# Optimization experiments

Measured on AMD Instinct MI355X. Metric: run time of the kernel, lower is better.

Reference implementation:

```python
import jax, jax.numpy as jnp
import numpy as np

NB = 32          # num_basis
RMAX = 2.5       # max_radius
M0, M1 = 16, 8   # multiplicities of 0e and 1o irreps

# normalize2mom constant for silu (makes E[act(x)^2]=1 under N(0,1)), as in e3nn FullyConnectedNet
_p, _w = np.polynomial.hermite_e.hermegauss(128)
_s = _p / (1.0 + np.exp(-_p))
SILU_C = float(1.0 / np.sqrt((_w * _s * _s).sum() / np.sqrt(2.0 * np.pi)))

INV3 = 1.0 / np.sqrt(3.0)   # w3j(1,1,0)=w3j(0,1,1)=w3j(1,0,1) coefficient
INV6 = 1.0 / np.sqrt(6.0)   # w3j(1,1,1) = eps_ijk/sqrt(6)
PW0 = float(np.sqrt(1.0 / (M0 + M1)))        # path weight -> 0e (component/element norm)
PW1 = float(np.sqrt(3.0 / (M0 + M1 + M1)))   # path weight -> 1o
PW_SIM = float(np.sqrt(1.0 / (M0 * M0 + M1 * M1)))  # similarity TP path weight


def basis_net(rb, W1, W2):
    # e3nn FullyConnectedNet([NB,16,numel], silu): x@W/sqrt(fan_in), normalized act, linear out
    h = SILU_C * jax.nn.silu(rb @ (W1 / np.sqrt(NB)))
    return h @ (W2 / np.sqrt(16.0))


def fc_tp(x0, x1, sh0, sh1, w):
    # FullyConnectedTensorProduct (16x0e+8x1o) x (0e+1o) -> (16x0e+8x1o), per-edge weights
    # x0 [E,16], x1 [E,8,3], sh0 [E], sh1 [E,3], w [E,640]
    E = w.shape[0]
    w0 = w[:, 0:256].reshape(E, M0, M0)    # 0e x 0e -> 0e
    w1 = w[:, 256:384].reshape(E, M0, M1)  # 0e x 1o -> 1o
    w2 = w[:, 384:448].reshape(E, M1, M1)  # 1o x 0e -> 1o
    w3 = w[:, 448:576].reshape(E, M1, M0)  # 1o x 1o -> 0e
    w4 = w[:, 576:640].reshape(E, M1, M1)  # 1o x 1o -> 1o
    dot = jnp.einsum('eui,ei->eu', x1, sh1)
    out0 = PW0 * (jnp.einsum('euw,eu->ew', w0, x0 * sh0[:, None])
                  + INV3 * jnp.einsum('euw,eu->ew', w3, dot))
    crx = jnp.cross(x1, sh1[:, None, :])
    out1 = PW1 * (INV3 * jnp.einsum('euw,eu,ei->ewi', w1, x0, sh1)
                  + INV3 * sh0[:, None, None] * jnp.einsum('euw,eui->ewi', w2, x1)
                  + INV6 * jnp.einsum('euw,eui->ewi', w4, crx))
    return out0, out1


def forward(x, pos, edge_src, edge_dst, w_key1, w_key2, w_val1, w_val2, w_q0, w_q1, w_sim0, w_sim1):
    N = x.shape[0]
    x0 = x[:, :M0]                       # [N,16] scalars
    x1 = x[:, M0:].reshape(N, M1, 3)     # [N,8,3] vectors
    vec = pos[edge_src] - pos[edge_dst]  # [E,3]
    r = jnp.sqrt((vec * vec).sum(-1) + 1e-12)
    # bessel soft_one_hot_linspace with cutoff, scaled by sqrt(num_basis)
    n = jnp.arange(1, NB + 1, dtype=x.dtype) * jnp.pi
    rb = jnp.sqrt(2.0 / RMAX) * jnp.sin(n * (r[:, None] / RMAX)) / r[:, None]
    rb = jnp.where(r[:, None] < RMAX, rb, 0.0) * np.sqrt(1.0 * NB)
    # spherical harmonics lmax=1, normalize=True, normalization='component'
    unit = vec / r[:, None]
    sh0 = jnp.ones_like(r)
    sh1 = np.sqrt(3.0) * unit
    # query projection (o3.Linear, per-irrep dense / sqrt(fan_in))
    q0 = x0 @ (w_q0 / np.sqrt(M0))
    q1 = jnp.einsum('nui,uv->nvi', x1, w_q1) / np.sqrt(M1)
    x0s, x1s = x0[edge_src], x1[edge_src]
    k0, k1 = fc_tp(x0s, x1s, sh0, sh1, basis_net(rb, w_key1, w_key2))
    v0, v1 = fc_tp(x0s, x1s, sh0, sh1, basis_net(rb, w_val1, w_val2))
    # similarity TP (q,k)->0e
    s = PW_SIM * (jnp.einsum('eu,uv,ev->e', q0[edge_dst], w_sim0, k0)
                  + INV3 * jnp.einsum('eui,uv,evi->e', q1[edge_dst], w_sim1, k1))
    # scatter softmax over incoming edges per dst node
    smax = jax.ops.segment_max(s, edge_dst, num_segments=N)
    ex = jnp.exp(s - smax[edge_dst])
    attn = ex / jax.ops.segment_sum(ex, edge_dst, num_segments=N)[edge_dst]
    coef = jnp.sqrt(jax.nn.relu(attn))
    vals = jnp.concatenate([v0, v1.reshape(-1, 3 * M1)], axis=-1)  # [E,40]
    return jax.ops.segment_sum(coef[:, None] * vals, edge_dst, num_segments=N)


def setup_inputs() -> dict:
    key = jax.random.key(0)
    ks = jax.random.split(key, 12)
    N, E = 16384, 262144
    return dict(
        x=jax.random.normal(ks[0], (N, 40), jnp.float32),
        pos=jax.random.uniform(ks[1], (N, 3), jnp.float32) * 2.0,  # box so r spans cutoff
        edge_src=jax.random.randint(ks[2], (E,), 0, N, jnp.int32),
        edge_dst=jax.random.randint(ks[3], (E,), 0, N, jnp.int32),
        w_key1=jax.random.normal(ks[4], (32, 16), jnp.float32),
        w_key2=jax.random.normal(ks[5], (16, 640), jnp.float32),
        w_val1=jax.random.normal(ks[6], (32, 16), jnp.float32),
        w_val2=jax.random.normal(ks[7], (16, 640), jnp.float32),
        w_q0=jax.random.normal(ks[8], (16, 16), jnp.float32),
        w_q1=jax.random.normal(ks[9], (8, 8), jnp.float32),
        w_sim0=jax.random.normal(ks[10], (16, 16), jnp.float32),
        w_sim1=jax.random.normal(ks[11], (8, 8), jnp.float32),
    )


def reference(x, pos, edge_src, edge_dst, w_key1, w_key2, w_val1, w_val2, w_q0, w_q1, w_sim0, w_sim1):
    return forward(x, pos, edge_src, edge_dst, w_key1, w_key2, w_val1, w_val2, w_q0, w_q1, w_sim0, w_sim1)
```

## Files before the change

### kernel.cpp

```cpp
#include <hip/hip_runtime.h>
#include <math.h>

#define TPB 256
#define TPBF 192
#define SRCS_PER_GRP 8
#define SRC_STRIDE_U16 1928

#define RMAX_F 2.5f
#define PI_F 3.14159265358979323846f
#define SQRT3_F 1.7320508075688772f
#define INV3_F 0.5773502691896258f
#define INV6_F 0.4082482904638631f
#define PW0_F 0.2041241452319315f
#define PW1_F 0.3061862178478972f
#define PWSIM_F 0.05590169943749474f
#define SILU_C_F 1.676866f
#define RB_F 0.8944271909999159f
#define INV_SQRT8_F 0.35355339059327373f

typedef unsigned short u16t;
typedef _Float16 f16x2 __attribute__((ext_vector_type(2)));

#if defined(__has_builtin)
#if __has_builtin(__builtin_amdgcn_fdot2)
#define HAVE_FDOT2 1
#else
#define HAVE_FDOT2 0
#endif
#else
#define HAVE_FDOT2 0
#endif


__device__ __forceinline__ unsigned f2bf(float f) {
  unsigned b = __float_as_uint(f);
  return (b + 0x7fffu + ((b >> 16) & 1u)) >> 16;
}
__device__ __forceinline__ float bf2f(unsigned s) {
  return __uint_as_float(s << 16);
}

__device__ __forceinline__ f16x2 as_f16x2(int v) {
  union { int i; f16x2 h; } u; u.i = v; return u.h;
}

__device__ __forceinline__ float dot2f16(f16x2 a, f16x2 b, float c) {
#if HAVE_FDOT2
  return __builtin_amdgcn_fdot2(a, b, c, false);
#else
  return fmaf((float)a.x, (float)b.x, fmaf((float)a.y, (float)b.y, c));
#endif
}

__device__ __forceinline__ float dotjh(const u16t* __restrict__ t,
                                       const f16x2* __restrict__ hp) {
  const int4* q = reinterpret_cast<const int4*>(t);
  int4 a = q[0], b = q[1];
  float s0 = 0.f, s1 = 0.f;
  s0 = dot2f16(as_f16x2(a.x), hp[0], s0);
  s1 = dot2f16(as_f16x2(a.y), hp[1], s1);
  s0 = dot2f16(as_f16x2(a.z), hp[2], s0);
  s1 = dot2f16(as_f16x2(a.w), hp[3], s1);
  s0 = dot2f16(as_f16x2(b.x), hp[4], s0);
  s1 = dot2f16(as_f16x2(b.y), hp[5], s1);
  s0 = dot2f16(as_f16x2(b.z), hp[6], s0);
  s1 = dot2f16(as_f16x2(b.w), hp[7], s1);
  return s0 + s1;
}

__device__ __forceinline__ void pack_h16(const float* __restrict__ h,
                                         f16x2* __restrict__ hp) {
#pragma unroll
  for (int i = 0; i < 8; ++i) {
    f16x2 v;
    v.x = (_Float16)h[2 * i + 0];
    v.y = (_Float16)h[2 * i + 1];
    hp[i] = v;
  }
}

__device__ __forceinline__ float dot16u(const float* __restrict__ w, const float* __restrict__ h) {
  float a0 = 0.f, a1 = 0.f, a2 = 0.f, a3 = 0.f;
#pragma unroll
  for (int j = 0; j < 16; j += 4) {
    a0 = fmaf(h[j + 0], w[j + 0], a0);
    a1 = fmaf(h[j + 1], w[j + 1], a1);
    a2 = fmaf(h[j + 2], w[j + 2], a2);
    a3 = fmaf(h[j + 3], w[j + 3], a3);
  }
  return (a0 + a1) + (a2 + a3);
}

__device__ __forceinline__ void compute_h2s(const float* __restrict__ pos,
                                            const float* __restrict__ W1k,
                                            const float* __restrict__ W1v,
                                            int src, int dst,
                                            float& shx, float& shy, float& shz,
                                            float hk[16], float hv[16]) {
  float vx = pos[3 * src + 0] - pos[3 * dst + 0];
  float vy = pos[3 * src + 1] - pos[3 * dst + 1];
  float vz = pos[3 * src + 2] - pos[3 * dst + 2];
  float r2 = fmaf(vx, vx, fmaf(vy, vy, vz * vz)) + 1e-12f;
  float r = sqrtf(r2);
  float inv_r = 1.0f / r;
  shx = SQRT3_F * vx * inv_r;
  shy = SQRT3_F * vy * inv_r;
  shz = SQRT3_F * vz * inv_r;
  float f = (r < RMAX_F) ? (RB_F * inv_r) : 0.0f;
  float t0 = (PI_F / RMAX_F) * r;
  float s1, c1;
  __sincosf(t0, &s1, &c1);
  float c2 = 2.0f * c1;
  float sm = 0.0f, sc = s1;
  float ak[16], av[16];
#pragma unroll
  for (int j = 0; j < 16; ++j) { ak[j] = 0.0f; av[j] = 0.0f; }
#pragma unroll 2
  for (int n = 0; n < 32; ++n) {
    float rb = f * sc;
    const float* wk = W1k + n * 16;
    const float* wv = W1v + n * 16;
#pragma unroll
    for (int j = 0; j < 16; ++j) ak[j] = fmaf(rb, wk[j], ak[j]);
#pragma unroll
    for (int j = 0; j < 16; ++j) av[j] = fmaf(rb, wv[j], av[j]);
    float nx = fmaf(c2, sc, -sm);
    sm = sc; sc = nx;
  }
#pragma unroll
  for (int j = 0; j < 16; ++j) {
    float v = ak[j];
    hk[j] = SILU_C_F * v * (1.0f / (1.0f + __expf(-v)));
    float w = av[j];
    hv[j] = SILU_C_F * w * (1.0f / (1.0f + __expf(-w)));
  }
}

__device__ __forceinline__ void gen_entry(const float* __restrict__ W2T,
                                          const float* __restrict__ xr,
                                          int mm, float out[16]) {
#pragma unroll
  for (int j = 0; j < 16; ++j) out[j] = 0.f;
  if (mm < 16) {
    int w = mm;
#pragma unroll 1
    for (int u = 0; u < 16; ++u) {
      float xu = xr[u];
      const float* wp = W2T + (u * 16 + w) * 16;
#pragma unroll
      for (int j = 0; j < 16; ++j) out[j] = fmaf(xu, wp[j], out[j]);
    }
  } else if (mm < 24) {
    int w = mm - 16;
#pragma unroll 1
    for (int u = 0; u < 16; ++u) {
      float xu = xr[u];
      const float* wp = W2T + (256 + u * 8 + w) * 16;
#pragma unroll
      for (int j = 0; j < 16; ++j) out[j] = fmaf(xu, wp[j], out[j]);
    }
  } else if (mm < 48) {
    int tt = mm - 24, w = tt / 3, i = tt - w * 3;
#pragma unroll 1
    for (int u = 0; u < 8; ++u) {
      float xu = xr[16 + u * 3 + i];
      const float* wp = W2T + (384 + u * 8 + w) * 16;
#pragma unroll
      for (int j = 0; j < 16; ++j) out[j] = fmaf(xu, wp[j], out[j]);
    }
  } else if (mm < 96) {
    int tt = mm - 48, w = tt / 3, i = tt - w * 3;
#pragma unroll 1
    for (int u = 0; u < 8; ++u) {
      float xu = xr[16 + u * 3 + i];
      const float* wp = W2T + (448 + u * 16 + w) * 16;
#pragma unroll
      for (int j = 0; j < 16; ++j) out[j] = fmaf(xu, wp[j], out[j]);
    }
  } else {
    int tt = mm - 96, w = tt / 3, i = tt - w * 3;
#pragma unroll 1
    for (int u = 0; u < 8; ++u) {
      float xu = xr[16 + u * 3 + i];
      const float* wp = W2T + (576 + u * 8 + w) * 16;
#pragma unroll
      for (int j = 0; j < 16; ++j) out[j] = fmaf(xu, wp[j], out[j]);
    }
  }
}

__device__ __forceinline__ void gen_tables(const float* __restrict__ W2T,
                                           const float* __restrict__ xsh,
                                           u16t* __restrict__ tl,
                                           int nsrc, int tid) {
  for (int idx = tid; idx < nsrc * 120; idx += TPBF) {
    int m, s;
    if (nsrc == SRCS_PER_GRP) {
      m = idx >> 3;
      s = idx & 7;
    } else {
      m = idx / nsrc;
      s = idx - m * nsrc;
    }
    float out[16];
    gen_entry(W2T, xsh + s * 40, m, out);
    unsigned r[8];
#pragma unroll
    for (int k = 0; k < 8; ++k) {
      union { f16x2 h; unsigned u; } cv;
      cv.h.x = (_Float16)out[2 * k + 0];
      cv.h.y = (_Float16)out[2 * k + 1];
      r[k] = cv.u;
    }
    int4* dp = reinterpret_cast<int4*>(&tl[s * SRC_STRIDE_U16 + m * 16]);
    dp[0] = make_int4((int)r[0], (int)r[1], (int)r[2], (int)r[3]);
    dp[1] = make_int4((int)r[4], (int)r[5], (int)r[6], (int)r[7]);
  }
}


__global__ void k_prep(const float* __restrict__ wk2, const float* __restrict__ wv2,
                       const float* __restrict__ wq0, const float* __restrict__ wq1,
                       const float* __restrict__ ws0, const float* __restrict__ ws1,
                       float* __restrict__ W2Tk, float* __restrict__ W2Tv,
                       float* __restrict__ C0, float* __restrict__ C1) {
  int i = blockIdx.x * blockDim.x + threadIdx.x;
  if (i < 10240) {
    int o = i >> 4, j = i & 15;
    W2Tk[i] = wk2[j * 640 + o] * 0.25f;
  } else if (i < 20480) {
    int k = i - 10240;
    int o = k >> 4, j = k & 15;
    W2Tv[k] = wv2[j * 640 + o] * 0.25f;
  } else if (i < 20736) {
    int k = i - 20480;
    int t = k >> 4, v = k & 15;
    float a = 0.f;
#pragma unroll
    for (int u = 0; u < 16; ++u) a = fmaf(wq0[t * 16 + u] * 0.25f, ws0[u * 16 + v], a);
    C0[k] = a;
  } else if (i < 20800) {
    int k = i - 20736;
    int t = k >> 3, v = k & 7;
    float a = 0.f;
#pragma unroll
    for (int u = 0; u < 8; ++u) a = fmaf(wq1[t * 8 + u] * INV_SQRT8_F, ws1[u * 8 + v], a);
    C1[k] = a;
  }
}

__global__ void k_node(const float* __restrict__ x, const float* __restrict__ C0,
                       const float* __restrict__ C1, float* __restrict__ qs0g,
                       float* __restrict__ qs1g, int N) {
  int n = blockIdx.x * blockDim.x + threadIdx.x;
  if (n >= N) return;
  float xr[40];
  const float4* p = reinterpret_cast<const float4*>(x + (size_t)n * 40);
#pragma unroll
  for (int q = 0; q < 10; ++q) {
    float4 v = p[q];
    xr[q * 4 + 0] = v.x; xr[q * 4 + 1] = v.y; xr[q * 4 + 2] = v.z; xr[q * 4 + 3] = v.w;
  }
  float o0[16];
#pragma unroll
  for (int v = 0; v < 16; ++v) o0[v] = 0.f;
#pragma unroll
  for (int t = 0; t < 16; ++t) {
    float xt = xr[t];
    const float* c = C0 + t * 16;
#pragma unroll
    for (int v = 0; v < 16; ++v) o0[v] = fmaf(xt, c[v], o0[v]);
  }
  float4* q0p = reinterpret_cast<float4*>(qs0g + (size_t)n * 16);
#pragma unroll
  for (int q = 0; q < 4; ++q)
    q0p[q] = make_float4(o0[q * 4], o0[q * 4 + 1], o0[q * 4 + 2], o0[q * 4 + 3]);

  float o1[24];
#pragma unroll
  for (int v = 0; v < 24; ++v) o1[v] = 0.f;
#pragma unroll
  for (int u = 0; u < 8; ++u) {
    const float* c = C1 + u * 8;
    float xa = xr[16 + u * 3 + 0], xb = xr[16 + u * 3 + 1], xc = xr[16 + u * 3 + 2];
#pragma unroll
    for (int v = 0; v < 8; ++v) {
      float cv = c[v];
      o1[v * 3 + 0] = fmaf(xa, cv, o1[v * 3 + 0]);
      o1[v * 3 + 1] = fmaf(xb, cv, o1[v * 3 + 1]);
      o1[v * 3 + 2] = fmaf(xc, cv, o1[v * 3 + 2]);
    }
  }
  float4* q1p = reinterpret_cast<float4*>(qs1g + (size_t)n * 24);
#pragma unroll
  for (int q = 0; q < 6; ++q)
    q1p[q] = make_float4(o1[q * 4], o1[q * 4 + 1], o1[q * 4 + 2], o1[q * 4 + 3]);
}


__global__ void k_hist2(const int* __restrict__ esrc, const int* __restrict__ edst,
                        int* __restrict__ cnt_s, int* __restrict__ cnt_d, int E) {
  int e = blockIdx.x * blockDim.x + threadIdx.x;
  if (e < E) {
    atomicAdd(&cnt_s[esrc[e]], 1);
    atomicAdd(&cnt_d[edst[e]], 1);
  }
}

__global__ void k_hist1(const int* __restrict__ key, int* __restrict__ cnt, int E) {
  int e = blockIdx.x * blockDim.x + threadIdx.x;
  if (e < E) atomicAdd(&cnt[key[e]], 1);
}

__global__ __launch_bounds__(1024) void k_scan2(const int* __restrict__ cnt_s,
                                                int* __restrict__ off_s,
                                                int* __restrict__ cur_s,
                                                const int* __restrict__ cnt_d,
                                                int* __restrict__ off_d,
                                                int* __restrict__ cur_d, int N) {
  const int* __restrict__ cnt = blockIdx.x ? cnt_d : cnt_s;
  int* __restrict__ off = blockIdx.x ? off_d : off_s;
  int* __restrict__ cur = blockIdx.x ? cur_d : cur_s;
  __shared__ int ls[1024];
  int tid = threadIdx.x;
  int per = (N + 1023) >> 10;
  int base = tid * per;
  int sum = 0;
  for (int j = 0; j < per; ++j) {
    int idx = base + j;
    if (idx < N) sum += cnt[idx];
  }
  ls[tid] = sum;
  __syncthreads();
  for (int d = 1; d < 1024; d <<= 1) {
    int v = (tid >= d) ? ls[tid - d] : 0;
    __syncthreads();
    ls[tid] += v;
    __syncthreads();
  }
  int run = ls[tid] - sum;
  for (int j = 0; j < per; ++j) {
    int idx = base + j;
    if (idx < N) {
      off[idx] = run;
      cur[idx] = run;
      run += cnt[idx];
    }
  }
  if (tid == 1023) off[N] = run;
}

__global__ void k_place(const int* __restrict__ key, int* __restrict__ cursor,
                        int* __restrict__ perm, int E) {
  int e = blockIdx.x * blockDim.x + threadIdx.x;
  if (e < E) {
    int p = atomicAdd(&cursor[key[e]], 1);
    perm[p] = e;
  }
}

__global__ void k_idx_dst(const int* __restrict__ perm, const int* __restrict__ edst,
                          int* __restrict__ cursor, int* __restrict__ idx, int E) {
  int p = blockIdx.x * blockDim.x + threadIdx.x;
  if (p < E) {
    int q = atomicAdd(&cursor[edst[perm[p]]], 1);
    idx[q] = p;
  }
}


__global__ __launch_bounds__(TPBF) void k_fused(
    const float* __restrict__ x, const float* __restrict__ pos,
    const int* __restrict__ esrc, const int* __restrict__ edst,
    const int* __restrict__ perm, const int* __restrict__ off_s,
    const float* __restrict__ W1k, const float* __restrict__ W2Tk,
    const float* __restrict__ W1v, const float* __restrict__ W2Tv,
    const float* __restrict__ qs0g, const float* __restrict__ qs1g,
    float* __restrict__ s_out, u16t* __restrict__ stg, int N) {
  __shared__ __align__(16) u16t tl[SRCS_PER_GRP * SRC_STRIDE_U16];
  __shared__ float xsh[SRCS_PER_GRP * 40];
  int tid = threadIdx.x;
  int base = blockIdx.x * SRCS_PER_GRP;
  int nsrc = min(SRCS_PER_GRP, N - base);
  int glo = off_s[base], ghi = off_s[base + nsrc];

  for (int idx = tid; idx < nsrc * 40; idx += TPBF) {
    int s = idx / 40, u = idx - s * 40;
    xsh[s * 40 + u] = x[(size_t)(base + s) * 40 + u];
  }
  __syncthreads();

  gen_tables(W2Tk, xsh, tl, nsrc, tid);
  __syncthreads();

  for (int p0 = glo; p0 < ghi; p0 += TPBF) {
    int p = p0 + tid;
    bool act = p < ghi;

    float shx = 0.f, shy = 0.f, shz = 0.f;
    int sloc = 0;
    f16x2 hvp[8];
#pragma unroll
    for (int j = 0; j < 8; ++j) { hvp[j].x = (_Float16)0.f; hvp[j].y = (_Float16)0.f; }

    if (act) {
      int e = perm[p];
      int src = esrc[e];
      int dst = edst[e];
      sloc = src - base;
      float hk[16], hv[16];
      compute_h2s(pos, W1k, W1v, src, dst, shx, shy, shz, hk, hv);
      f16x2 hkp[8];
      pack_h16(hk, hkp);
      pack_h16(hv, hvp);

      const u16t* tk = &tl[sloc * SRC_STRIDE_U16];
      const float4* q0p = reinterpret_cast<const float4*>(qs0g + (size_t)dst * 16);
      float S0 = 0.f;
#pragma unroll 1
      for (int w4 = 0; w4 < 4; ++w4) {
        float4 qq = q0p[w4];
        float q[4] = {qq.x, qq.y, qq.z, qq.w};
#pragma unroll
        for (int k = 0; k < 4; ++k) {
          float t0 = dotjh(tk + (w4 * 4 + k) * 16, hkp);
          float t3x = dotjh(tk + (48 + w4 * 12 + k * 3 + 0) * 16, hkp);
          float t3y = dotjh(tk + (48 + w4 * 12 + k * 3 + 1) * 16, hkp);
          float t3z = dotjh(tk + (48 + w4 * 12 + k * 3 + 2) * 16, hkp);
          S0 = fmaf(q[k], fmaf(INV3_F, t3x * shx + t3y * shy + t3z * shz, t0), S0);
        }
      }
      const float4* q1p = reinterpret_cast<const float4*>(qs1g + (size_t)dst * 24);
      float S1 = 0.f;
#pragma unroll 1
      for (int w4 = 0; w4 < 2; ++w4) {
        float4 qa = q1p[w4 * 3 + 0];
        float4 qb = q1p[w4 * 3 + 1];
        float4 qc = q1p[w4 * 3 + 2];
        float q[12] = {qa.x, qa.y, qa.z, qa.w, qb.x, qb.y, qb.z, qb.w,
                       qc.x, qc.y, qc.z, qc.w};
#pragma unroll
        for (int k = 0; k < 4; ++k) {
          float qx = q[k * 3 + 0], qy = q[k * 3 + 1], qz = q[k * 3 + 2];
          float t1 = dotjh(tk + (16 + w4 * 4 + k) * 16, hkp);
          float t2x = dotjh(tk + (24 + w4 * 12 + k * 3 + 0) * 16, hkp);
          float t2y = dotjh(tk + (24 + w4 * 12 + k * 3 + 1) * 16, hkp);
          float t2z = dotjh(tk + (24 + w4 * 12 + k * 3 + 2) * 16, hkp);
          float c0 = dotjh(tk + (96 + w4 * 12 + k * 3 + 0) * 16, hkp);
          float c1 = dotjh(tk + (96 + w4 * 12 + k * 3 + 1) * 16, hkp);
          float c2 = dotjh(tk + (96 + w4 * 12 + k * 3 + 2) * 16, hkp);
          float crx = c1 * shz - c2 * shy;
          float cry = c2 * shx - c0 * shz;
          float crz = c0 * shy - c1 * shx;
          float qdots = qx * shx + qy * shy + qz * shz;
          S1 += INV3_F * (t1 * qdots + t2x * qx + t2y * qy + t2z * qz) +
                INV6_F * (crx * qx + cry * qy + crz * qz);
        }
      }
      s_out[p] = PWSIM_F * (PW0_F * S0 + PW1_F * INV3_F * S1);
    }
    __syncthreads();

    gen_tables(W2Tv, xsh, tl, nsrc, tid);
    __syncthreads();

    if (act) {
      const u16t* tv = &tl[sloc * SRC_STRIDE_U16];
      u16t* sp = stg + (size_t)p * 40;
#pragma unroll 1
      for (int w4 = 0; w4 < 4; ++w4) {
        float f[4];
#pragma unroll
        for (int k = 0; k < 4; ++k) {
          float t0 = dotjh(tv + (w4 * 4 + k) * 16, hvp);
          float t3x = dotjh(tv + (48 + w4 * 12 + k * 3 + 0) * 16, hvp);
          float t3y = dotjh(tv + (48 + w4 * 12 + k * 3 + 1) * 16, hvp);
          float t3z = dotjh(tv + (48 + w4 * 12 + k * 3 + 2) * 16, hvp);
          f[k] = PW0_F * fmaf(INV3_F, t3x * shx + t3y * shy + t3z * shz, t0);
        }
        int2 pk;
        pk.x = (int)(f2bf(f[0]) | (f2bf(f[1]) << 16));
        pk.y = (int)(f2bf(f[2]) | (f2bf(f[3]) << 16));
        *reinterpret_cast<int2*>(sp + w4 * 4) = pk;
      }
#pragma unroll 1
      for (int w4 = 0; w4 < 2; ++w4) {
        float f[12];
#pragma unroll
        for (int k = 0; k < 4; ++k) {
          float t1 = dotjh(tv + (16 + w4 * 4 + k) * 16, hvp);
          float t2x = dotjh(tv + (24 + w4 * 12 + k * 3 + 0) * 16, hvp);
          float t2y = dotjh(tv + (24 + w4 * 12 + k * 3 + 1) * 16, hvp);
          float t2z = dotjh(tv + (24 + w4 * 12 + k * 3 + 2) * 16, hvp);
          float c0 = dotjh(tv + (96 + w4 * 12 + k * 3 + 0) * 16, hvp);
          float c1 = dotjh(tv + (96 + w4 * 12 + k * 3 + 1) * 16, hvp);
          float c2 = dotjh(tv + (96 + w4 * 12 + k * 3 + 2) * 16, hvp);
          float crx = c1 * shz - c2 * shy;
          float cry = c2 * shx - c0 * shz;
          float crz = c0 * shy - c1 * shx;
          f[k * 3 + 0] = PW1_F * (INV3_F * fmaf(t1, shx, t2x) + INV6_F * crx);
          f[k * 3 + 1] = PW1_F * (INV3_F * fmaf(t1, shy, t2y) + INV6_F * cry);
          f[k * 3 + 2] = PW1_F * (INV3_F * fmaf(t1, shz, t2z) + INV6_F * crz);
        }
#pragma unroll
        for (int g = 0; g < 3; ++g) {
          int2 pk;
          pk.x = (int)(f2bf(f[g * 4 + 0]) | (f2bf(f[g * 4 + 1]) << 16));
          pk.y = (int)(f2bf(f[g * 4 + 2]) | (f2bf(f[g * 4 + 3]) << 16));
          *reinterpret_cast<int2*>(sp + 16 + w4 * 12 + g * 4) = pk;
        }
      }
    }

    if (p0 + TPBF < ghi) {
      __syncthreads();
      gen_tables(W2Tk, xsh, tl, nsrc, tid);
      __syncthreads();
    }
  }
}


__global__ void k_smg(const float* __restrict__ s, const u16t* __restrict__ stg,
                      const int* __restrict__ off, const int* __restrict__ idx,
                      float* __restrict__ out, int N) {
  int gid = blockIdx.x * blockDim.x + threadIdx.x;
  int wid = gid >> 6;
  int lane = threadIdx.x & 63;
  if (wid >= N) return;
  int lo = off[wid], hi = off[wid + 1];
  float m = -1e30f;
  for (int q = lo + lane; q < hi; q += 64) m = fmaxf(m, s[idx[q]]);
#pragma unroll
  for (int d = 32; d; d >>= 1) m = fmaxf(m, __shfl_xor(m, d));
  float sum = 0.f;
  for (int q = lo + lane; q < hi; q += 64) sum += __expf(s[idx[q]] - m);
#pragma unroll
  for (int d = 32; d; d >>= 1) sum += __shfl_xor(sum, d);
  float inv = 1.0f / sum;
  if (lane < 40) {
    float acc = 0.f;
    for (int q = lo; q < hi; ++q) {
      int p = idx[q];
      float c = sqrtf(__expf(s[p] - m) * inv);
      acc = fmaf(c, bf2f((unsigned)stg[(size_t)p * 40 + lane]), acc);
    }
    out[(size_t)wid * 40 + lane] = acc;
  }
}


__global__ __launch_bounds__(TPB) void k_edge_fused(
    const float* __restrict__ x, const float* __restrict__ pos,
    const int* __restrict__ esrc, const int* __restrict__ edst,
    const int* __restrict__ perm,
    const float* __restrict__ W1k, const float* __restrict__ W2Tk,
    const float* __restrict__ W1v, const float* __restrict__ W2Tv,
    const float* __restrict__ qs0g, const float* __restrict__ qs1g,
    float* __restrict__ s_out, float* __restrict__ staging, int E) {
  __shared__ float xs[TPB * 41];
  int p = blockIdx.x * TPB + threadIdx.x;
  if (p >= E) return;
  int e = perm[p];
  int src = esrc[e], dst = edst[e];

  float* myx = &xs[threadIdx.x * 41];
  const float4* xrow = reinterpret_cast<const float4*>(x + (size_t)src * 40);
#pragma unroll
  for (int q = 0; q < 10; ++q) {
    float4 v = xrow[q];
    myx[q * 4 + 0] = v.x; myx[q * 4 + 1] = v.y; myx[q * 4 + 2] = v.z; myx[q * 4 + 3] = v.w;
  }

  float sh1[3], hk[16], hv[16];
  compute_h2s(pos, W1k, W1v, src, dst, sh1[0], sh1[1], sh1[2], hk, hv);

  {
    float qs0[16];
    {
      const float4* qp = reinterpret_cast<const float4*>(qs0g + (size_t)dst * 16);
#pragma unroll
      for (int q = 0; q < 4; ++q) {
        float4 v = qp[q];
        qs0[q * 4 + 0] = v.x; qs0[q * 4 + 1] = v.y; qs0[q * 4 + 2] = v.z; qs0[q * 4 + 3] = v.w;
      }
    }
    float qs1[24];
    {
      const float4* qp = reinterpret_cast<const float4*>(qs1g + (size_t)dst * 24);
#pragma unroll
      for (int q = 0; q < 6; ++q) {
        float4 v = qp[q];
        qs1[q * 4 + 0] = v.x; qs1[q * 4 + 1] = v.y; qs1[q * 4 + 2] = v.z; qs1[q * 4 + 3] = v.w;
      }
    }
    float qsh[8];
#pragma unroll
    for (int w = 0; w < 8; ++w)
      qsh[w] = qs1[w * 3] * sh1[0] + qs1[w * 3 + 1] * sh1[1] + qs1[w * 3 + 2] * sh1[2];

    float S0a = 0.f, S0b = 0.f, S1a = 0.f, S1b = 0.f, S1c = 0.f;
#pragma unroll 1
    for (int u = 0; u < 16; ++u) {
      const float* base = W2Tk + (u * 16) * 16;
      float accu = 0.f;
#pragma unroll
      for (int w = 0; w < 16; ++w) accu = fmaf(dot16u(base + w * 16, hk), qs0[w], accu);
      S0a = fmaf(accu, myx[u], S0a);
    }
#pragma unroll 1
    for (int u = 0; u < 16; ++u) {
      const float* base = W2Tk + (256 + u * 8) * 16;
      float accu = 0.f;
#pragma unroll
      for (int w = 0; w < 8; ++w) accu = fmaf(dot16u(base + w * 16, hk), qsh[w], accu);
      S1a = fmaf(accu, myx[u], S1a);
    }
#pragma unroll 1
    for (int u = 0; u < 8; ++u) {
      const float* base = W2Tk + (384 + u * 8) * 16;
      float x1a = myx[16 + u * 3 + 0], x1b = myx[16 + u * 3 + 1], x1c = myx[16 + u * 3 + 2];
      float accu = 0.f;
#pragma unroll
      for (int w = 0; w < 8; ++w) {
        float t = qs1[w * 3] * x1a + qs1[w * 3 + 1] * x1b + qs1[w * 3 + 2] * x1c;
        accu = fmaf(dot16u(base + w * 16, hk), t, accu);
      }
      S1b += accu;
    }
#pragma unroll 1
    for (int u = 0; u < 8; ++u) {
      const float* base = W2Tk + (448 + u * 16) * 16;
      float x1a = myx[16 + u * 3 + 0], x1b = myx[16 + u * 3 + 1], x1c = myx[16 + u * 3 + 2];
      float du = x1a * sh1[0] + x1b * sh1[1] + x1c * sh1[2];
      float accu = 0.f;
#pragma unroll
      for (int w = 0; w < 16; ++w) accu = fmaf(dot16u(base + w * 16, hk), qs0[w], accu);
      S0b = fmaf(accu, du, S0b);
    }
#pragma unroll 1
    for (int u = 0; u < 8; ++u) {
      const float* base = W2Tk + (576 + u * 8) * 16;
      float x1a = myx[16 + u * 3 + 0], x1b = myx[16 + u * 3 + 1], x1c = myx[16 + u * 3 + 2];
      float cx = x1b * sh1[2] - x1c * sh1[1];
      float cy = x1c * sh1[0] - x1a * sh1[2];
      float cz = x1a * sh1[1] - x1b * sh1[0];
      float accu = 0.f;
#pragma unroll
      for (int w = 0; w < 8; ++w) {
        float t = qs1[w * 3] * cx + qs1[w * 3 + 1] * cy + qs1[w * 3 + 2] * cz;
        accu = fmaf(dot16u(base + w * 16, hk), t, accu);
      }
      S1c += accu;
    }
    s_out[p] = PWSIM_F * (PW0_F * (S0a + INV3_F * S0b) +
                          (INV3_F * PW1_F) * (INV3_F * S1a + INV3_F * S1b + INV6_F * S1c));
  }

  float v0[16];
#pragma unroll
  for (int w = 0; w < 16; ++w) v0[w] = 0.f;
  float v1[24];
#pragma unroll
  for (int w = 0; w < 24; ++w) v1[w] = 0.f;

#pragma unroll 1
  for (int u = 0; u < 16; ++u) {
    const float* base = W2Tv + (u * 16) * 16;
    float xu = myx[u];
#pragma unroll
    for (int w = 0; w < 16; ++w) v0[w] = fmaf(dot16u(base + w * 16, hv), xu, v0[w]);
  }
  {
    float aw[8];
#pragma unroll
    for (int w = 0; w < 8; ++w) aw[w] = 0.f;
#pragma unroll 1
    for (int u = 0; u < 16; ++u) {
      const float* base = W2Tv + (256 + u * 8) * 16;
      float xu = myx[u];
#pragma unroll
      for (int w = 0; w < 8; ++w) aw[w] = fmaf(dot16u(base + w * 16, hv), xu, aw[w]);
    }
#pragma unroll
    for (int w = 0; w < 8; ++w) {
      float t = INV3_F * aw[w];
      v1[w * 3 + 0] = fmaf(t, sh1[0], v1[w * 3 + 0]);
      v1[w * 3 + 1] = fmaf(t, sh1[1], v1[w * 3 + 1]);
      v1[w * 3 + 2] = fmaf(t, sh1[2], v1[w * 3 + 2]);
    }
  }
#pragma unroll 1
  for (int u = 0; u < 8; ++u) {
    const float* base = W2Tv + (384 + u * 8) * 16;
    float a0 = INV3_F * myx[16 + u * 3 + 0];
    float a1 = INV3_F * myx[16 + u * 3 + 1];
    float a2 = INV3_F * myx[16 + u * 3 + 2];
#pragma unroll
    for (int w = 0; w < 8; ++w) {
      float wk = dot16u(base + w * 16, hv);
      v1[w * 3 + 0] = fmaf(wk, a0, v1[w * 3 + 0]);
      v1[w * 3 + 1] = fmaf(wk, a1, v1[w * 3 + 1]);
      v1[w * 3 + 2] = fmaf(wk, a2, v1[w * 3 + 2]);
    }
  }
#pragma unroll 1
  for (int u = 0; u < 8; ++u) {
    const float* base = W2Tv + (448 + u * 16) * 16;
    float x1a = myx[16 + u * 3 + 0], x1b = myx[16 + u * 3 + 1], x1c = myx[16 + u * 3 + 2];
    float du = INV3_F * (x1a * sh1[0] + x1b * sh1[1] + x1c * sh1[2]);
#pragma unroll
    for (int w = 0; w < 16; ++w) v0[w] = fmaf(dot16u(base + w * 16, hv), du, v0[w]);
  }
#pragma unroll 1
  for (int u = 0; u < 8; ++u) {
    const float* base = W2Tv + (576 + u * 8) * 16;
    float x1a = myx[16 + u * 3 + 0], x1b = myx[16 + u * 3 + 1], x1c = myx[16 + u * 3 + 2];
    float cx = INV6_F * (x1b * sh1[2] - x1c * sh1[1]);
    float cy = INV6_F * (x1c * sh1[0] - x1a * sh1[2]);
    float cz = INV6_F * (x1a * sh1[1] - x1b * sh1[0]);
#pragma unroll
    for (int w = 0; w < 8; ++w) {
      float wk = dot16u(base + w * 16, hv);
      v1[w * 3 + 0] = fmaf(wk, cx, v1[w * 3 + 0]);
      v1[w * 3 + 1] = fmaf(wk, cy, v1[w * 3 + 1]);
      v1[w * 3 + 2] = fmaf(wk, cz, v1[w * 3 + 2]);
    }
  }

  float outv[40];
#pragma unroll
  for (int w = 0; w < 16; ++w) outv[w] = PW0_F * v0[w];
#pragma unroll
  for (int w = 0; w < 24; ++w) outv[16 + w] = PW1_F * v1[w];
  float4* st = reinterpret_cast<float4*>(staging + (size_t)p * 40);
#pragma unroll
  for (int q = 0; q < 10; ++q)
    st[q] = make_float4(outv[q * 4], outv[q * 4 + 1], outv[q * 4 + 2], outv[q * 4 + 3]);
}

__global__ void k_softmax(const float* __restrict__ s, const int* __restrict__ off,
                          float* __restrict__ coef, int N) {
  int gid = blockIdx.x * blockDim.x + threadIdx.x;
  int wid = gid >> 6;
  int lane = threadIdx.x & 63;
  if (wid >= N) return;
  int lo = off[wid], hi = off[wid + 1];
  float m = -1e30f;
  for (int p = lo + lane; p < hi; p += 64) m = fmaxf(m, s[p]);
#pragma unroll
  for (int d = 32; d; d >>= 1) m = fmaxf(m, __shfl_xor(m, d));
  float sum = 0.f;
  for (int p = lo + lane; p < hi; p += 64) sum += __expf(s[p] - m);
#pragma unroll
  for (int d = 32; d; d >>= 1) sum += __shfl_xor(sum, d);
  float inv = 1.0f / sum;
  for (int p = lo + lane; p < hi; p += 64)
    coef[p] = sqrtf(__expf(s[p] - m) * inv);
}

__global__ void k_gather(const float* __restrict__ staging, const float* __restrict__ coef,
                         const int* __restrict__ off, float* __restrict__ out, int N) {
  int gid = blockIdx.x * blockDim.x + threadIdx.x;
  int wid = gid >> 6;
  int lane = threadIdx.x & 63;
  if (wid >= N) return;
  int lo = off[wid], hi = off[wid + 1];
  if (lane < 40) {
    float acc = 0.f;
    for (int p = lo; p < hi; ++p)
      acc = fmaf(coef[p], staging[(size_t)p * 40 + lane], acc);
    out[(size_t)wid * 40 + lane] = acc;
  }
}


extern "C" void kernel_launch(void* const* d_in, const int* in_sizes, int n_in,
                              void* d_out, int out_size, void* d_ws, size_t ws_size,
                              hipStream_t stream) {
  const float* x   = (const float*)d_in[0];
  const float* pos = (const float*)d_in[1];
  const int* esrc  = (const int*)d_in[2];
  const int* edst  = (const int*)d_in[3];
  const float* wk1 = (const float*)d_in[4];
  const float* wk2 = (const float*)d_in[5];
  const float* wv1 = (const float*)d_in[6];
  const float* wv2 = (const float*)d_in[7];
  const float* wq0 = (const float*)d_in[8];
  const float* wq1 = (const float*)d_in[9];
  const float* ws0 = (const float*)d_in[10];
  const float* ws1 = (const float*)d_in[11];

  int E = in_sizes[2];
  int N = in_sizes[0] / 40;

  float* ws = (float*)d_ws;
  float* W2Tk = ws;
  float* W2Tv = ws + 10240;
  float* C0   = ws + 20480;
  float* C1   = ws + 20736;
  float* qs0g = ws + 20800;
  float* qs1g = qs0g + (size_t)N * 16;
  float* base2 = qs1g + (size_t)N * 24;

  float* s_ws = base2;
  int* cnt_s  = (int*)(s_ws + (size_t)E);
  int* cnt_d  = cnt_s + N;
  int* off_s  = cnt_d + N;
  int* cur_s  = off_s + N + 1;
  int* off_d  = cur_s + N;
  int* cur_d  = off_d + N + 1;
  int* perm   = cur_d + N;
  int* idxd   = perm + (size_t)E;
  u16t* stgb  = (u16t*)(idxd + (size_t)E);
  size_t need_fast = (size_t)((char*)(stgb + (size_t)E * 40) - (char*)d_ws);

  k_prep<<<(20800 + 255) / 256, 256, 0, stream>>>(wk2, wv2, wq0, wq1, ws0, ws1,
                                                  W2Tk, W2Tv, C0, C1);
  k_node<<<(N + 255) / 256, 256, 0, stream>>>(x, C0, C1, qs0g, qs1g, N);

  if (ws_size >= need_fast) {
    hipMemsetAsync(cnt_s, 0, sizeof(int) * (size_t)(2 * N), stream);
    k_hist2<<<(E + 255) / 256, 256, 0, stream>>>(esrc, edst, cnt_s, cnt_d, E);
    k_scan2<<<2, 1024, 0, stream>>>(cnt_s, off_s, cur_s, cnt_d, off_d, cur_d, N);
    k_place<<<(E + 255) / 256, 256, 0, stream>>>(esrc, cur_s, perm, E);
    k_idx_dst<<<(E + 255) / 256, 256, 0, stream>>>(perm, edst, cur_d, idxd, E);
    int ng = (N + SRCS_PER_GRP - 1) / SRCS_PER_GRP;
    k_fused<<<ng, TPBF, 0, stream>>>(x, pos, esrc, edst, perm, off_s,
                                     wk1, W2Tk, wv1, W2Tv, qs0g, qs1g,
                                     s_ws, stgb, N);
    k_smg<<<((N * 64) + 255) / 256, 256, 0, stream>>>(s_ws, stgb, off_d, idxd,
                                                      (float*)d_out, N);
  } else {
    float* coefF = s_ws + (size_t)E;
    int* cnt    = (int*)(coefF + (size_t)E);
    int* off    = cnt + N;
    int* cursor = off + N + 1;
    int* permF  = cursor + N;
    float* staging = (float*)(permF + (size_t)E);

    hipMemsetAsync(cnt, 0, sizeof(int) * (size_t)N, stream);
    k_hist1<<<(E + 255) / 256, 256, 0, stream>>>(edst, cnt, E);
    k_scan2<<<1, 1024, 0, stream>>>(cnt, off, cursor, cnt, off, cursor, N);
    k_place<<<(E + 255) / 256, 256, 0, stream>>>(edst, cursor, permF, E);
    k_edge_fused<<<(E + TPB - 1) / TPB, TPB, 0, stream>>>(
        x, pos, esrc, edst, permF, wk1, W2Tk, wv1, W2Tv, qs0g, qs1g,
        s_ws, staging, E);
    k_softmax<<<((N * 64) + 255) / 256, 256, 0, stream>>>(s_ws, off, coefF, N);
    k_gather<<<((N * 64) + 255) / 256, 256, 0, stream>>>(staging, coefF, off,
                                                         (float*)d_out, N);
  }
}
```

Baseline: 276.7 us.

## Generate per-source weight tables with packed fp16 math and merge placement kernels

Table generation in the fused edge kernel now reads fp16 copies of the transposed second-layer weights and accumulates with packed half2 multiply-adds. Node features are staged in shared memory as duplicated half pairs instead of floats. This is meant to halve weight-load bandwidth and double ALU throughput in the table-building phase, at the cost of accumulating in fp16, which risks more rounding error. Separately, the source-placement and destination-index kernels are merged into one launch. Because the destination order is now assigned from the original edge order rather than in sorted-source order, the per-destination ordering of summed terms may differ.

```diff
diff --git a/kernel.cpp b/kernel.cpp
--- a/kernel.cpp
+++ b/kernel.cpp
@@ -42,6 +42,9 @@
 
 __device__ __forceinline__ f16x2 as_f16x2(int v) {
   union { int i; f16x2 h; } u; u.i = v; return u.h;
+}
+__device__ __forceinline__ unsigned f16x2_bits(f16x2 h) {
+  union { f16x2 h; unsigned u; } c; c.h = h; return c.u;
 }
 
 __device__ __forceinline__ float dot2f16(f16x2 a, f16x2 b, float c) {
@@ -136,61 +139,64 @@
   }
 }
 
-__device__ __forceinline__ void gen_entry(const float* __restrict__ W2T,
-                                          const float* __restrict__ xr,
-                                          int mm, float out[16]) {
-#pragma unroll
-  for (int j = 0; j < 16; ++j) out[j] = 0.f;
+__device__ __forceinline__ void gen_entry_h(const u16t* __restrict__ W2H,
+                                            const unsigned* __restrict__ xh,
+                                            int mm, unsigned outw[8]) {
+  f16x2 acc[8];
+#pragma unroll
+  for (int i = 0; i < 8; ++i) { acc[i].x = (_Float16)0.f; acc[i].y = (_Float16)0.f; }
   if (mm < 16) {
     int w = mm;
 #pragma unroll 1
     for (int u = 0; u < 16; ++u) {
-      float xu = xr[u];
-      const float* wp = W2T + (u * 16 + w) * 16;
-#pragma unroll
-      for (int j = 0; j < 16; ++j) out[j] = fmaf(xu, wp[j], out[j]);
+      f16x2 xv = as_f16x2((int)xh[u]);
+      const f16x2* wp = reinterpret_cast<const f16x2*>(W2H + (u * 16 + w) * 16);
+#pragma unroll
+      for (int i = 0; i < 8; ++i) acc[i] += xv * wp[i];
     }
   } else if (mm < 24) {
     int w = mm - 16;
 #pragma unroll 1
     for (int u = 0; u < 16; ++u) {
-      float xu = xr[u];
-      const float* wp = W2T + (256 + u * 8 + w) * 16;
-#pragma unroll
-      for (int j = 0; j < 16; ++j) out[j] = fmaf(xu, wp[j], out[j]);
+      f16x2 xv = as_f16x2((int)xh[u]);
+      const f16x2* wp = reinterpret_cast<const f16x2*>(W2H + (256 + u * 8 + w) * 16);
+#pragma unroll
+      for (int i = 0; i < 8; ++i) acc[i] += xv * wp[i];
     }
   } else if (mm < 48) {
-    int tt = mm - 24, w = tt / 3, i = tt - w * 3;
+    int tt = mm - 24, w = tt / 3, i3 = tt - w * 3;
 #pragma unroll 1
     for (int u = 0; u < 8; ++u) {
-      float xu = xr[16 + u * 3 + i];
-      const float* wp = W2T + (384 + u * 8 + w) * 16;
-#pragma unroll
-      for (int j = 0; j < 16; ++j) out[j] = fmaf(xu, wp[j], out[j]);
+      f16x2 xv = as_f16x2((int)xh[16 + u * 3 + i3]);
+      const f16x2* wp = reinterpret_cast<const f16x2*>(W2H + (384 + u * 8 + w) * 16);
+#pragma unroll
+      for (int i = 0; i < 8; ++i) acc[i] += xv * wp[i];
     }
   } else if (mm < 96) {
-    int tt = mm - 48, w = tt / 3, i = tt - w * 3;
+    int tt = mm - 48, w = tt / 3, i3 = tt - w * 3;
 #pragma unroll 1
     for (int u = 0; u < 8; ++u) {
-      float xu = xr[16 + u * 3 + i];
-      const float* wp = W2T + (448 + u * 16 + w) * 16;
-#pragma unroll
-      for (int j = 0; j < 16; ++j) out[j] = fmaf(xu, wp[j], out[j]);
+      f16x2 xv = as_f16x2((int)xh[16 + u * 3 + i3]);
+      const f16x2* wp = reinterpret_cast<const f16x2*>(W2H + (448 + u * 16 + w) * 16);
+#pragma unroll
+      for (int i = 0; i < 8; ++i) acc[i] += xv * wp[i];
     }
   } else {
-    int tt = mm - 96, w = tt / 3, i = tt - w * 3;
+    int tt = mm - 96, w = tt / 3, i3 = tt - w * 3;
 #pragma unroll 1
     for (int u = 0; u < 8; ++u) {
-      float xu = xr[16 + u * 3 + i];
-      const float* wp = W2T + (576 + u * 8 + w) * 16;
-#pragma unroll
-      for (int j = 0; j < 16; ++j) out[j] = fmaf(xu, wp[j], out[j]);
-    }
-  }
-}
-
-__device__ __forceinline__ void gen_tables(const float* __restrict__ W2T,
-                                           const float* __restrict__ xsh,
+      f16x2 xv = as_f16x2((int)xh[16 + u * 3 + i3]);
+      const f16x2* wp = reinterpret_cast<const f16x2*>(W2H + (576 + u * 8 + w) * 16);
+#pragma unroll
+      for (int i = 0; i < 8; ++i) acc[i] += xv * wp[i];
+    }
+  }
+#pragma unroll
+  for (int i = 0; i < 8; ++i) outw[i] = f16x2_bits(acc[i]);
+}
+
+__device__ __forceinline__ void gen_tables(const u16t* __restrict__ W2H,
+                                           const unsigned* __restrict__ xh,
                                            u16t* __restrict__ tl,
                                            int nsrc, int tid) {
   for (int idx = tid; idx < nsrc * 120; idx += TPBF) {
@@ -202,16 +208,8 @@
       m = idx / nsrc;
       s = idx - m * nsrc;
     }
-    float out[16];
-    gen_entry(W2T, xsh + s * 40, m, out);
     unsigned r[8];
-#pragma unroll
-    for (int k = 0; k < 8; ++k) {
-      union { f16x2 h; unsigned u; } cv;
-      cv.h.x = (_Float16)out[2 * k + 0];
-      cv.h.y = (_Float16)out[2 * k + 1];
-      r[k] = cv.u;
-    }
+    gen_entry_h(W2H, xh + s * 40, m, r);
     int4* dp = reinterpret_cast<int4*>(&tl[s * SRC_STRIDE_U16 + m * 16]);
     dp[0] = make_int4((int)r[0], (int)r[1], (int)r[2], (int)r[3]);
     dp[1] = make_int4((int)r[4], (int)r[5], (int)r[6], (int)r[7]);
@@ -223,15 +221,22 @@
                        const float* __restrict__ wq0, const float* __restrict__ wq1,
                        const float* __restrict__ ws0, const float* __restrict__ ws1,
                        float* __restrict__ W2Tk, float* __restrict__ W2Tv,
+                       u16t* __restrict__ W2Hk, u16t* __restrict__ W2Hv,
                        float* __restrict__ C0, float* __restrict__ C1) {
   int i = blockIdx.x * blockDim.x + threadIdx.x;
   if (i < 10240) {
     int o = i >> 4, j = i & 15;
-    W2Tk[i] = wk2[j * 640 + o] * 0.25f;
+    float v = wk2[j * 640 + o] * 0.25f;
+    W2Tk[i] = v;
+    union { _Float16 h; u16t u; } c; c.h = (_Float16)v;
+    W2Hk[i] = c.u;
   } else if (i < 20480) {
     int k = i - 10240;
     int o = k >> 4, j = k & 15;
-    W2Tv[k] = wv2[j * 640 + o] * 0.25f;
+    float v = wv2[j * 640 + o] * 0.25f;
+    W2Tv[k] = v;
+    union { _Float16 h; u16t u; } c; c.h = (_Float16)v;
+    W2Hv[k] = c.u;
   } else if (i < 20736) {
     int k = i - 20480;
     int t = k >> 4, v = k & 15;
@@ -350,6 +355,18 @@
   if (tid == 1023) off[N] = run;
 }
 
+__global__ void k_place2(const int* __restrict__ esrc, const int* __restrict__ edst,
+                         int* __restrict__ cur_s, int* __restrict__ cur_d,
+                         int* __restrict__ perm, int* __restrict__ idx, int E) {
+  int e = blockIdx.x * blockDim.x + threadIdx.x;
+  if (e < E) {
+    int p = atomicAdd(&cur_s[esrc[e]], 1);
+    perm[p] = e;
+    int q = atomicAdd(&cur_d[edst[e]], 1);
+    idx[q] = p;
+  }
+}
+
 __global__ void k_place(const int* __restrict__ key, int* __restrict__ cursor,
                         int* __restrict__ perm, int E) {
   int e = blockIdx.x * blockDim.x + threadIdx.x;
@@ -359,26 +376,17 @@
   }
 }
 
-__global__ void k_idx_dst(const int* __restrict__ perm, const int* __restrict__ edst,
-                          int* __restrict__ cursor, int* __restrict__ idx, int E) {
-  int p = blockIdx.x * blockDim.x + threadIdx.x;
-  if (p < E) {
-    int q = atomicAdd(&cursor[edst[perm[p]]], 1);
-    idx[q] = p;
-  }
-}
-
 
 __global__ __launch_bounds__(TPBF) void k_fused(
     const float* __restrict__ x, const float* __restrict__ pos,
     const int* __restrict__ esrc, const int* __restrict__ edst,
     const int* __restrict__ perm, const int* __restrict__ off_s,
-    const float* __restrict__ W1k, const float* __restrict__ W2Tk,
-    const float* __restrict__ W1v, const float* __restrict__ W2Tv,
+    const float* __restrict__ W1k, const u16t* __restrict__ W2Hk,
+    const float* __restrict__ W1v, const u16t* __restrict__ W2Hv,
     const float* __restrict__ qs0g, const float* __restrict__ qs1g,
     float* __restrict__ s_out, u16t* __restrict__ stg, int N) {
   __shared__ __align__(16) u16t tl[SRCS_PER_GRP * SRC_STRIDE_U16];
-  __shared__ float xsh[SRCS_PER_GRP * 40];
+  __shared__ unsigned xh[SRCS_PER_GRP * 40];
   int tid = threadIdx.x;
   int base = blockIdx.x * SRCS_PER_GRP;
   int nsrc = min(SRCS_PER_GRP, N - base);
@@ -386,11 +394,13 @@
 
   for (int idx = tid; idx < nsrc * 40; idx += TPBF) {
     int s = idx / 40, u = idx - s * 40;
-    xsh[s * 40 + u] = x[(size_t)(base + s) * 40 + u];
+    float v = x[(size_t)(base + s) * 40 + u];
+    f16x2 hh; hh.x = (_Float16)v; hh.y = hh.x;
+    xh[s * 40 + u] = f16x2_bits(hh);
   }
   __syncthreads();
 
-  gen_tables(W2Tk, xsh, tl, nsrc, tid);
+  gen_tables(W2Hk, xh, tl, nsrc, tid);
   __syncthreads();
 
   for (int p0 = glo; p0 < ghi; p0 += TPBF) {
@@ -461,7 +471,7 @@
     }
     __syncthreads();
 
-    gen_tables(W2Tv, xsh, tl, nsrc, tid);
+    gen_tables(W2Hv, xh, tl, nsrc, tid);
     __syncthreads();
 
     if (act) {
@@ -514,7 +524,7 @@
 
     if (p0 + TPBF < ghi) {
       __syncthreads();
-      gen_tables(W2Tk, xsh, tl, nsrc, tid);
+      gen_tables(W2Hk, xh, tl, nsrc, tid);
       __syncthreads();
     }
   }
@@ -799,7 +809,9 @@
   float* W2Tv = ws + 10240;
   float* C0   = ws + 20480;
   float* C1   = ws + 20736;
-  float* qs0g = ws + 20800;
+  u16t* W2Hk  = (u16t*)(ws + 20800);
+  u16t* W2Hv  = W2Hk + 10240;
+  float* qs0g = ws + 20800 + 10240;
   float* qs1g = qs0g + (size_t)N * 16;
   float* base2 = qs1g + (size_t)N * 24;
 
@@ -816,18 +828,18 @@
   size_t need_fast = (size_t)((char*)(stgb + (size_t)E * 40) - (char*)d_ws);
 
   k_prep<<<(20800 + 255) / 256, 256, 0, stream>>>(wk2, wv2, wq0, wq1, ws0, ws1,
-                                                  W2Tk, W2Tv, C0, C1);
+                                                  W2Tk, W2Tv, W2Hk, W2Hv, C0, C1);
   k_node<<<(N + 255) / 256, 256, 0, stream>>>(x, C0, C1, qs0g, qs1g, N);
 
   if (ws_size >= need_fast) {
     hipMemsetAsync(cnt_s, 0, sizeof(int) * (size_t)(2 * N), stream);
     k_hist2<<<(E + 255) / 256, 256, 0, stream>>>(esrc, edst, cnt_s, cnt_d, E);
     k_scan2<<<2, 1024, 0, stream>>>(cnt_s, off_s, cur_s, cnt_d, off_d, cur_d, N);
-    k_place<<<(E + 255) / 256, 256, 0, stream>>>(esrc, cur_s, perm, E);
-    k_idx_dst<<<(E + 255) / 256, 256, 0, stream>>>(perm, edst, cur_d, idxd, E);
+    k_place2<<<(E + 255) / 256, 256, 0, stream>>>(esrc, edst, cur_s, cur_d,
+                                                  perm, idxd, E);
     int ng = (N + SRCS_PER_GRP - 1) / SRCS_PER_GRP;
     k_fused<<<ng, TPBF, 0, stream>>>(x, pos, esrc, edst, perm, off_s,
-                                     wk1, W2Tk, wv1, W2Tv, qs0g, qs1g,
+                                     wk1, W2Hk, wv1, W2Hv, qs0g, qs1g,
                                      s_ws, stgb, N);
     k_smg<<<((N * 64) + 255) / 256, 256, 0, stream>>>(s_ws, stgb, off_d, idxd,
                                                       (float*)d_out, N);
```

After: 263.6 us. 1.05x faster.
